# Optimization experiments

Hardware: AMD Instinct MI355X
Metric: run time of the kernel (lower is better)

Reference implementation:

```python
import jax, jax.numpy as jnp
import numpy as np

HIDDEN = 2048
NUM_HEADS = 32
NUM_KV_HEADS = 8
HEAD_DIM = 64
ROPE_THETA = 10000.0


def _rope_tables(S, dtype=jnp.float32):
    freqs = 1.0 / (ROPE_THETA ** (jnp.arange(0, HEAD_DIM, 2, dtype=jnp.float32) / HEAD_DIM))
    angles = jnp.arange(S, dtype=jnp.float32)[:, None] * freqs[None, :]  # [S, D/2]
    return jnp.cos(angles).astype(dtype), jnp.sin(angles).astype(dtype)


def _apply_rope(x, cos, sin):
    # x: [B, H, S, D] with interleaved even/odd rotation pairs
    xe = x[..., 0::2]
    xo = x[..., 1::2]
    oe = xe * cos - xo * sin
    oo = xe * sin + xo * cos
    return jnp.stack([oe, oo], axis=-1).reshape(x.shape)


def setup_inputs() -> dict:
    key = jax.random.key(0)
    ks = jax.random.split(key, 5)
    scale = 0.02
    return {
        "x": jax.random.normal(ks[0], (2, 2048, HIDDEN), dtype=jnp.float32),
        "wq": jax.random.normal(ks[1], (NUM_HEADS * HEAD_DIM, HIDDEN), dtype=jnp.float32) * scale,
        "wk": jax.random.normal(ks[2], (NUM_KV_HEADS * HEAD_DIM, HIDDEN), dtype=jnp.float32) * scale,
        "wv": jax.random.normal(ks[3], (NUM_KV_HEADS * HEAD_DIM, HIDDEN), dtype=jnp.float32) * scale,
        "wo": jax.random.normal(ks[4], (HIDDEN, NUM_HEADS * HEAD_DIM), dtype=jnp.float32) * scale,
    }


def reference(x, wq, wk, wv, wo):
    B, S, _ = x.shape
    G = NUM_HEADS // NUM_KV_HEADS  # GQA group size

    q = (x @ wq.T).reshape(B, S, NUM_HEADS, HEAD_DIM).transpose(0, 2, 1, 3)      # [B,Hq,S,D]
    k = (x @ wk.T).reshape(B, S, NUM_KV_HEADS, HEAD_DIM).transpose(0, 2, 1, 3)   # [B,Hkv,S,D]
    v = (x @ wv.T).reshape(B, S, NUM_KV_HEADS, HEAD_DIM).transpose(0, 2, 1, 3)

    cos, sin = _rope_tables(S, x.dtype)
    q = _apply_rope(q, cos, sin)
    k = _apply_rope(k, cos, sin)

    # GQA without materializing repeated K/V: fold group dim into q
    qg = q.reshape(B, NUM_KV_HEADS, G, S, HEAD_DIM)
    scale = 1.0 / jnp.sqrt(jnp.asarray(HEAD_DIM, dtype=x.dtype))
    scores = jnp.einsum("bkgsd,bktd->bkgst", qg, k) * scale  # [B,Hkv,G,S,S]

    causal = jnp.tril(jnp.ones((S, S), dtype=bool))
    scores = jnp.where(causal, scores, jnp.finfo(scores.dtype).min)
    probs = jax.nn.softmax(scores, axis=-1)

    out = jnp.einsum("bkgst,bktd->bkgsd", probs, v)                 # [B,Hkv,G,S,D]
    out = out.reshape(B, NUM_HEADS, S, HEAD_DIM).transpose(0, 2, 1, 3).reshape(B, S, NUM_HEADS * HEAD_DIM)
    return out @ wo.T
```

## Files before the change

### kernel.cpp

```cpp
#include <hip/hip_runtime.h>
#include <hip/hip_bf16.h>

typedef __hip_bfloat16 bf16;
typedef __attribute__((ext_vector_type(8))) short short8;
typedef __attribute__((ext_vector_type(4))) float f32x4;

#define S_LEN 2048
#define BATCH 2
#define M_TOT 4096
#define HID 2048
#define NH 32
#define NKV 8
#define HD 64
#define KVD 512

#define MFMA16(a, b, c) __builtin_amdgcn_mfma_f32_16x16x32_bf16(a, b, c, 0, 0, 0)

__device__ __forceinline__ void gload_lds16(const bf16* g, bf16* l) {
    __builtin_amdgcn_global_load_lds((const __attribute__((address_space(1))) void*)g,
                                     (__attribute__((address_space(3))) void*)l,
                                     16, 0, 0);
}

__device__ __forceinline__ float b2f(short v) {
    unsigned u = ((unsigned)(unsigned short)v) << 16;
    float f; __builtin_memcpy(&f, &u, 4); return f;
}

__global__ void cast_kernel(const float* __restrict__ src, bf16* __restrict__ dst, int n8) {
    int stride = gridDim.x * blockDim.x;
    for (int i = blockIdx.x * blockDim.x + threadIdx.x; i < n8; i += stride) {
        const float4* s = (const float4*)(src + (size_t)i * 8);
        float4 a = s[0], b = s[1];
        bf16 tmp[8];
        tmp[0] = __float2bfloat16(a.x); tmp[1] = __float2bfloat16(a.y);
        tmp[2] = __float2bfloat16(a.z); tmp[3] = __float2bfloat16(a.w);
        tmp[4] = __float2bfloat16(b.x); tmp[5] = __float2bfloat16(b.y);
        tmp[6] = __float2bfloat16(b.z); tmp[7] = __float2bfloat16(b.w);
        *(short8*)(dst + (size_t)i * 8) = *(short8*)tmp;
    }
}

__global__ void rope_tables_kernel(float* __restrict__ cosb, float* __restrict__ sinb) {
    int idx = blockIdx.x * blockDim.x + threadIdx.x;
    if (idx >= S_LEN * 32) return;
    int s = idx >> 5, d = idx & 31;
    float freq = powf(10000.0f, -(float)(2 * d) / 64.0f);
    float ang = (float)s * freq;
    cosb[idx] = cosf(ang);
    sinb[idx] = sinf(ang);
}

__global__ void rope_kernel(bf16* __restrict__ buf, const float* __restrict__ cosb,
                            const float* __restrict__ sinb, int nh, int npairs) {
    int stride = gridDim.x * blockDim.x;
    int hw = nh * 32;
    for (int idx = blockIdx.x * blockDim.x + threadIdx.x; idx < npairs; idx += stride) {
        int m = idx / hw;
        int r = idx - m * hw;
        int h = r >> 5, d = r & 31;
        int s = m & (S_LEN - 1);
        float c = cosb[s * 32 + d], sn = sinb[s * 32 + d];
        bf16* p = buf + (size_t)m * (nh * HD) + h * HD + 2 * d;
        __hip_bfloat162 xv = *(__hip_bfloat162*)p;
        float xe = __bfloat162float(xv.x), xo = __bfloat162float(xv.y);
        __hip_bfloat162 ov;
        ov.x = __float2bfloat16(xe * c - xo * sn);
        ov.y = __float2bfloat16(xe * sn + xo * c);
        *(__hip_bfloat162*)p = ov;
    }
}

__device__ __forceinline__ short8 rope8(short8 v, float4 c, float4 s) {
    short8 o;
    const float* cp = (const float*)&c;
    const float* sp = (const float*)&s;
    #pragma unroll
    for (int m = 0; m < 4; m++) {
        float xe = b2f(v[2 * m]) * 0.125f;
        float xo = b2f(v[2 * m + 1]) * 0.125f;
        bf16 oe = __float2bfloat16(xe * cp[m] - xo * sp[m]);
        bf16 oo = __float2bfloat16(xe * sp[m] + xo * cp[m]);
        short se, so;
        __builtin_memcpy(&se, &oe, 2); __builtin_memcpy(&so, &oo, 2);
        o[2 * m] = se; o[2 * m + 1] = so;
    }
    return o;
}

__device__ __forceinline__ void gemm_core(const bf16* __restrict__ A,
                                          const bf16* __restrict__ W,
                                          int K, int m0, int n0,
                                          bf16* As, bf16* Bs,
                                          f32x4 acc[4][4]) {
    int tid = threadIdx.x;
    int lane = tid & 63, wid = tid >> 6;
    int wr = wid >> 1, wc = wid & 1;
    int lhi = lane >> 4, llo = lane & 15;
    const bf16* gA[4]; const bf16* gB[4];
    bf16 *lA[4], *lB[4];
    #pragma unroll
    for (int q = 0; q < 4; q++) {
        int c = tid + 256 * q;
        int row = c >> 3;
        int sl = (c & 7) ^ (row & 7);
        gA[q] = A + (size_t)(m0 + row) * K + sl * 8;
        gB[q] = W + (size_t)(n0 + row) * K + sl * 8;
        lA[q] = As + c * 8;
        lB[q] = Bs + c * 8;
    }
    for (int k0 = 0; k0 < K; k0 += 64) {
        #pragma unroll
        for (int q = 0; q < 4; q++) {
            gload_lds16(gA[q] + k0, lA[q]);
            gload_lds16(gB[q] + k0, lB[q]);
        }
        __syncthreads();
        short8 af[4][2], bfr[4][2];
        #pragma unroll
        for (int i = 0; i < 4; i++) {
            int row = wr * 64 + i * 16 + llo;
            int x = row & 7;
            af[i][0] = *(const short8*)(As + row * 64 + ((lhi ^ x) * 8));
            af[i][1] = *(const short8*)(As + row * 64 + (((4 + lhi) ^ x) * 8));
        }
        #pragma unroll
        for (int j = 0; j < 4; j++) {
            int row = wc * 64 + j * 16 + llo;
            int x = row & 7;
            bfr[j][0] = *(const short8*)(Bs + row * 64 + ((lhi ^ x) * 8));
            bfr[j][1] = *(const short8*)(Bs + row * 64 + (((4 + lhi) ^ x) * 8));
        }
        #pragma unroll
        for (int i = 0; i < 4; i++)
            #pragma unroll
            for (int j = 0; j < 4; j++) {
                acc[i][j] = MFMA16(af[i][0], bfr[j][0], acc[i][j]);
                acc[i][j] = MFMA16(af[i][1], bfr[j][1], acc[i][j]);
            }
        __syncthreads();
    }
}

__global__ __launch_bounds__(256) void gemm_qkv_kernel(
        const bf16* __restrict__ xb,
        const bf16* __restrict__ wq, const bf16* __restrict__ wk, const bf16* __restrict__ wv,
        bf16* __restrict__ qb, bf16* __restrict__ kb, bf16* __restrict__ vtb) {
    __shared__ bf16 As[128 * 64];
    __shared__ bf16 Bs[128 * 64];
    int by = blockIdx.y;
    const bf16* W; bf16* Cb; int n0, ldc, mode;
    if (by < 16)      { W = wq; Cb = qb;  n0 = by * 128;        ldc = 2048; mode = 0; }
    else if (by < 20) { W = wk; Cb = kb;  n0 = (by - 16) * 128; ldc = 512;  mode = 0; }
    else              { W = wv; Cb = vtb; n0 = (by - 20) * 128; ldc = 0;    mode = 1; }
    int m0 = blockIdx.x * 128;

    f32x4 acc[4][4] = {};
    gemm_core(xb, W, HID, m0, n0, As, Bs, acc);

    int lane = threadIdx.x & 63, wid = threadIdx.x >> 6;
    int wr = wid >> 1, wc = wid & 1;
    int lhi = lane >> 4, llo = lane & 15;
    #pragma unroll
    for (int i = 0; i < 4; i++)
        #pragma unroll
        for (int j = 0; j < 4; j++) {
            int col = wc * 64 + j * 16 + llo;
            #pragma unroll
            for (int r = 0; r < 4; r++) {
                int row = wr * 64 + i * 16 + lhi * 4 + r;
                int m = m0 + row;
                float v = acc[i][j][r];
                if (mode == 0) {
                    Cb[(size_t)m * ldc + n0 + col] = __float2bfloat16(v);
                } else {
                    int bb = m >> 11, ss = m & 2047;
                    Cb[((size_t)(bb * 512 + n0 + col)) * S_LEN + ss] = __float2bfloat16(v);
                }
            }
        }
}

__global__ __launch_bounds__(256) void gemm_out_kernel(
        const bf16* __restrict__ attnb, const bf16* __restrict__ wob,
        float* __restrict__ out) {
    __shared__ bf16 As[128 * 64];
    __shared__ bf16 Bs[128 * 64];
    int m0 = blockIdx.x * 128;
    int n0 = blockIdx.y * 128;
    f32x4 acc[4][4] = {};
    gemm_core(attnb, wob, HID, m0, n0, As, Bs, acc);

    int lane = threadIdx.x & 63, wid = threadIdx.x >> 6;
    int wr = wid >> 1, wc = wid & 1;
    int lhi = lane >> 4, llo = lane & 15;
    #pragma unroll
    for (int i = 0; i < 4; i++)
        #pragma unroll
        for (int j = 0; j < 4; j++) {
            int col = wc * 64 + j * 16 + llo;
            #pragma unroll
            for (int r = 0; r < 4; r++) {
                int row = wr * 64 + i * 16 + lhi * 4 + r;
                out[(size_t)(m0 + row) * HID + n0 + col] = acc[i][j][r];
            }
        }
}

__global__ __launch_bounds__(256, 4) void flash_kernel(
        const bf16* __restrict__ qb, const bf16* __restrict__ kb,
        const bf16* __restrict__ vtb, const float* __restrict__ cosb,
        const float* __restrict__ sinb, bf16* __restrict__ attnb) {
    __shared__ bf16 Ks[2][64 * 64];
    __shared__ bf16 Vs[2][64 * 64];
    __shared__ bf16 Pl[4][16 * 64];
    int bh = blockIdx.y;
    int b = bh >> 5, h = bh & 31;
    int kvh = h >> 2;
    int tid = threadIdx.x;
    int wid = tid >> 6, lane = tid & 63;
    int lhi = lane >> 4, llo = lane & 15;

    const bf16* Kg = kb + (size_t)(b * S_LEN) * KVD + kvh * HD;
    const bf16* Vg = vtb + (size_t)(b * 512 + kvh * 64) * S_LEN;

    int c0 = tid, c1 = tid + 256;
    int r0 = c0 >> 3, s0 = ((c0 & 7) ^ (r0 & 7)) * 8;
    int r1 = c1 >> 3, s1 = ((c1 & 7) ^ (r1 & 7)) * 8;

    bf16* pl = &Pl[wid][0];
    const int prd0 = llo * 64 + ((lhi ^ (llo & 7)) * 8);
    const int prd1 = llo * 64 + (((lhi + 4) ^ (llo & 7)) * 8);

    auto stage = [&](int buf, int t0) {
        gload_lds16(Kg + (size_t)(t0 + r0) * KVD + s0, &Ks[buf][c0 * 8]);
        gload_lds16(Kg + (size_t)(t0 + r1) * KVD + s1, &Ks[buf][c1 * 8]);
        gload_lds16(Vg + (size_t)r0 * S_LEN + t0 + s0, &Vs[buf][c0 * 8]);
        gload_lds16(Vg + (size_t)r1 * S_LEN + t0 + s1, &Vs[buf][c1 * 8]);
    };

    auto run_phase = [&](int j) {
        int qrow0 = j * 64 + wid * 16;
        int spos = qrow0 + llo;
        const bf16* qrow = qb + ((size_t)(b * S_LEN) + spos) * (NH * HD) + h * HD;
        float4 cv0 = *(const float4*)(cosb + spos * 32 + lhi * 4);
        float4 sv0 = *(const float4*)(sinb + spos * 32 + lhi * 4);
        float4 cv1 = *(const float4*)(cosb + spos * 32 + 16 + lhi * 4);
        float4 sv1 = *(const float4*)(sinb + spos * 32 + 16 + lhi * 4);
        short8 qf0 = rope8(*(const short8*)(qrow + lhi * 8), cv0, sv0);
        short8 qf1 = rope8(*(const short8*)(qrow + 32 + lhi * 8), cv1, sv1);

        f32x4 acc[4] = {};
        float psum[4] = {0.f, 0.f, 0.f, 0.f};

        stage(0, 0);
        asm volatile("s_waitcnt vmcnt(0)" ::: "memory");
        __builtin_amdgcn_s_barrier();
        int cur = 0;
        for (int t = 0; t <= j; ++t) {
            int t0 = t * 64;
            if (t < j) stage(cur ^ 1, t0 + 64);
            const bf16* Kc = &Ks[cur][0];
            const bf16* Vc = &Vs[cur][0];
            f32x4 z[4];
            #pragma unroll
            for (int cb = 0; cb < 4; cb++) {
                int row = cb * 16 + llo;
                int x = row & 7;
                short8 k0 = *(const short8*)(Kc + row * 64 + ((lhi ^ x) * 8));
                short8 k1 = *(const short8*)(Kc + row * 64 + (((lhi + 4) ^ x) * 8));
                f32x4 zz = {0.f, 0.f, 0.f, 0.f};
                zz = MFMA16(qf0, k0, zz);
                zz = MFMA16(qf1, k1, zz);
                z[cb] = zz;
            }
            if (t == j) {
                #pragma unroll
                for (int cb = 0; cb < 4; cb++)
                    #pragma unroll
                    for (int r = 0; r < 4; r++) {
                        float p = __expf(z[cb][r]);
                        p = (t0 + cb * 16 + llo <= qrow0 + lhi * 4 + r) ? p : 0.f;
                        psum[r] += p;
                        int row = lhi * 4 + r;
                        pl[row * 64 + (((2 * cb + (llo >> 3)) ^ (row & 7)) * 8) + (llo & 7)]
                            = __float2bfloat16(p);
                    }
            } else {
                #pragma unroll
                for (int cb = 0; cb < 4; cb++)
                    #pragma unroll
                    for (int r = 0; r < 4; r++) {
                        float p = __expf(z[cb][r]);
                        psum[r] += p;
                        int row = lhi * 4 + r;
                        pl[row * 64 + (((2 * cb + (llo >> 3)) ^ (row & 7)) * 8) + (llo & 7)]
                            = __float2bfloat16(p);
                    }
            }
            short8 pa0 = *(const short8*)(pl + prd0);
            short8 pa1 = *(const short8*)(pl + prd1);
            #pragma unroll
            for (int jb = 0; jb < 4; jb++) {
                int row = jb * 16 + llo;
                int x = row & 7;
                short8 v0 = *(const short8*)(Vc + row * 64 + ((lhi ^ x) * 8));
                short8 v1 = *(const short8*)(Vc + row * 64 + (((lhi + 4) ^ x) * 8));
                acc[jb] = MFMA16(pa0, v0, acc[jb]);
                acc[jb] = MFMA16(pa1, v1, acc[jb]);
            }
            asm volatile("s_waitcnt vmcnt(0)" ::: "memory");
            __builtin_amdgcn_s_barrier();
            cur ^= 1;
        }
        #pragma unroll
        for (int off = 1; off < 16; off <<= 1)
            #pragma unroll
            for (int r = 0; r < 4; r++)
                psum[r] += __shfl_xor(psum[r], off, 64);
        float inv[4];
        #pragma unroll
        for (int r = 0; r < 4; r++) inv[r] = 1.0f / psum[r];
        size_t obase = ((size_t)(b * S_LEN) + qrow0) * (NH * HD) + h * HD;
        #pragma unroll
        for (int jb = 0; jb < 4; jb++)
            #pragma unroll
            for (int r = 0; r < 4; r++)
                attnb[obase + (size_t)(lhi * 4 + r) * (NH * HD) + jb * 16 + llo] =
                    __float2bfloat16(acc[jb][r] * inv[r]);
    };

    run_phase(blockIdx.x);
    run_phase(31 - blockIdx.x);
}

extern "C" void kernel_launch(void* const* d_in, const int* in_sizes, int n_in,
                              void* d_out, int out_size, void* d_ws, size_t ws_size,
                              hipStream_t stream) {
    const float* x  = (const float*)d_in[0];
    const float* wq = (const float*)d_in[1];
    const float* wk = (const float*)d_in[2];
    const float* wv = (const float*)d_in[3];
    const float* wo = (const float*)d_in[4];
    float* out = (float*)d_out;

    char* ws = (char*)d_ws;
    size_t off = 0;
    auto alloc = [&](size_t bytes) { void* p = ws + off; off += (bytes + 255) & ~(size_t)255; return p; };
    bf16* xb   = (bf16*)alloc((size_t)M_TOT * HID * 2);
    bf16* wqb  = (bf16*)alloc((size_t)HID * HID * 2);
    bf16* wkb  = (bf16*)alloc((size_t)512 * HID * 2);
    bf16* wvb  = (bf16*)alloc((size_t)512 * HID * 2);
    bf16* wob  = (bf16*)alloc((size_t)HID * HID * 2);
    bf16* qb   = (bf16*)alloc((size_t)M_TOT * 2048 * 2);
    bf16* kb   = (bf16*)alloc((size_t)M_TOT * 512 * 2);
    bf16* vtb  = (bf16*)alloc((size_t)M_TOT * 512 * 2);
    bf16* attnb= (bf16*)alloc((size_t)M_TOT * 2048 * 2);
    float* cosb= (float*)alloc((size_t)S_LEN * 32 * 4);
    float* sinb= (float*)alloc((size_t)S_LEN * 32 * 4);

    auto cast = [&](const float* s, bf16* d, int n) {
        int n8 = n / 8;
        int grid = (n8 + 255) / 256;
        cast_kernel<<<grid, 256, 0, stream>>>(s, d, n8);
    };
    cast(x,  xb,  M_TOT * HID);
    cast(wq, wqb, HID * HID);
    cast(wk, wkb, 512 * HID);
    cast(wv, wvb, 512 * HID);
    cast(wo, wob, HID * HID);

    rope_tables_kernel<<<(S_LEN * 32 + 255) / 256, 256, 0, stream>>>(cosb, sinb);

    gemm_qkv_kernel<<<dim3(M_TOT / 128, 24), 256, 0, stream>>>(xb, wqb, wkb, wvb, qb, kb, vtb);

    {
        int npairs = M_TOT * NKV * 32;
        rope_kernel<<<(npairs + 255) / 256, 256, 0, stream>>>(kb, cosb, sinb, NKV, npairs);
    }

    flash_kernel<<<dim3(16, BATCH * NH), 256, 0, stream>>>(qb, kb, vtb, cosb, sinb, attnb);

    gemm_out_kernel<<<dim3(M_TOT / 128, HID / 128), 256, 0, stream>>>(attnb, wob, out);
}
```

Before: 211.9 us.

## Double-buffer GEMM K-loop, swizzle block order, fuse input casts into one kernel

The shared GEMM core now uses a K-step of 32 with two LDS buffers, issuing the next tile's global-to-LDS loads before the current tile's MFMAs. This overlaps memory latency with compute and leaves one barrier per step. Both GEMM kernels remap blockIdx.x so consecutive blocks walk strided M tiles, which changes cache locality. The five fp32-to-bf16 cast launches are merged into one grid-stride kernel writing into a contiguous workspace. That merge relies on the bf16 buffers being allocated contiguously with no alignment padding between them, and the smaller K-step doubles the number of loop iterations and barriers.

```diff
diff --git a/kernel.cpp b/kernel.cpp
--- a/kernel.cpp
+++ b/kernel.cpp
@@ -27,11 +27,23 @@
     float f; __builtin_memcpy(&f, &u, 4); return f;
 }
 
-__global__ void cast_kernel(const float* __restrict__ src, bf16* __restrict__ dst, int n8) {
+#define N8_X   1048576
+#define N8_WQ   524288
+#define N8_WK   131072
+#define N8_TOT 2359296
+__global__ void cast_all_kernel(const float* __restrict__ x, const float* __restrict__ wq,
+                                const float* __restrict__ wk, const float* __restrict__ wv,
+                                const float* __restrict__ wo, bf16* __restrict__ dst) {
     int stride = gridDim.x * blockDim.x;
-    for (int i = blockIdx.x * blockDim.x + threadIdx.x; i < n8; i += stride) {
-        const float4* s = (const float4*)(src + (size_t)i * 8);
-        float4 a = s[0], b = s[1];
+    for (int i = blockIdx.x * blockDim.x + threadIdx.x; i < N8_TOT; i += stride) {
+        const float* s; int off;
+        if (i < N8_X)                        { s = x;  off = i; }
+        else if (i < N8_X + N8_WQ)           { s = wq; off = i - N8_X; }
+        else if (i < N8_X + N8_WQ + N8_WK)   { s = wk; off = i - (N8_X + N8_WQ); }
+        else if (i < N8_X + N8_WQ + 2*N8_WK) { s = wv; off = i - (N8_X + N8_WQ + N8_WK); }
+        else                                 { s = wo; off = i - (N8_X + N8_WQ + 2*N8_WK); }
+        const float4* sp = (const float4*)(s + (size_t)off * 8);
+        float4 a = sp[0], b = sp[1];
         bf16 tmp[8];
         tmp[0] = __float2bfloat16(a.x); tmp[1] = __float2bfloat16(a.y);
         tmp[2] = __float2bfloat16(a.z); tmp[3] = __float2bfloat16(a.w);
@@ -97,48 +109,50 @@
     int lane = tid & 63, wid = tid >> 6;
     int wr = wid >> 1, wc = wid & 1;
     int lhi = lane >> 4, llo = lane & 15;
-    const bf16* gA[4]; const bf16* gB[4];
-    bf16 *lA[4], *lB[4];
-    #pragma unroll
-    for (int q = 0; q < 4; q++) {
-        int c = tid + 256 * q;
-        int row = c >> 3;
-        int sl = (c & 7) ^ (row & 7);
-        gA[q] = A + (size_t)(m0 + row) * K + sl * 8;
-        gB[q] = W + (size_t)(n0 + row) * K + sl * 8;
-        lA[q] = As + c * 8;
-        lB[q] = Bs + c * 8;
-    }
-    for (int k0 = 0; k0 < K; k0 += 64) {
-        #pragma unroll
-        for (int q = 0; q < 4; q++) {
-            gload_lds16(gA[q] + k0, lA[q]);
-            gload_lds16(gB[q] + k0, lB[q]);
-        }
-        __syncthreads();
-        short8 af[4][2], bfr[4][2];
+    int c0 = tid, c1 = tid + 256;
+    int r0 = c0 >> 2, s0 = ((c0 & 3) ^ (r0 & 3)) * 8;
+    int r1 = c1 >> 2, s1 = ((c1 & 3) ^ (r1 & 3)) * 8;
+    const bf16* gA0 = A + (size_t)(m0 + r0) * K + s0;
+    const bf16* gA1 = A + (size_t)(m0 + r1) * K + s1;
+    const bf16* gB0 = W + (size_t)(n0 + r0) * K + s0;
+    const bf16* gB1 = W + (size_t)(n0 + r1) * K + s1;
+
+    auto stage = [&](int buf, int k0) {
+        bf16* a = As + buf * 4096;
+        bf16* b = Bs + buf * 4096;
+        gload_lds16(gA0 + k0, a + c0 * 8);
+        gload_lds16(gA1 + k0, a + c1 * 8);
+        gload_lds16(gB0 + k0, b + c0 * 8);
+        gload_lds16(gB1 + k0, b + c1 * 8);
+    };
+
+    stage(0, 0);
+    asm volatile("s_waitcnt vmcnt(0)" ::: "memory");
+    __builtin_amdgcn_s_barrier();
+    int buf = 0;
+    for (int k0 = 0; k0 < K; k0 += 32) {
+        if (k0 + 32 < K) stage(buf ^ 1, k0 + 32);
+        const bf16* Ac = As + buf * 4096;
+        const bf16* Bc = Bs + buf * 4096;
+        short8 af[4], bfr[4];
         #pragma unroll
         for (int i = 0; i < 4; i++) {
             int row = wr * 64 + i * 16 + llo;
-            int x = row & 7;
-            af[i][0] = *(const short8*)(As + row * 64 + ((lhi ^ x) * 8));
-            af[i][1] = *(const short8*)(As + row * 64 + (((4 + lhi) ^ x) * 8));
+            af[i] = *(const short8*)(Ac + row * 32 + ((lhi ^ (row & 3)) * 8));
         }
         #pragma unroll
         for (int j = 0; j < 4; j++) {
             int row = wc * 64 + j * 16 + llo;
-            int x = row & 7;
-            bfr[j][0] = *(const short8*)(Bs + row * 64 + ((lhi ^ x) * 8));
-            bfr[j][1] = *(const short8*)(Bs + row * 64 + (((4 + lhi) ^ x) * 8));
+            bfr[j] = *(const short8*)(Bc + row * 32 + ((lhi ^ (row & 3)) * 8));
         }
         #pragma unroll
         for (int i = 0; i < 4; i++)
             #pragma unroll
-            for (int j = 0; j < 4; j++) {
-                acc[i][j] = MFMA16(af[i][0], bfr[j][0], acc[i][j]);
-                acc[i][j] = MFMA16(af[i][1], bfr[j][1], acc[i][j]);
-            }
-        __syncthreads();
+            for (int j = 0; j < 4; j++)
+                acc[i][j] = MFMA16(af[i], bfr[j], acc[i][j]);
+        asm volatile("s_waitcnt vmcnt(0)" ::: "memory");
+        __builtin_amdgcn_s_barrier();
+        buf ^= 1;
     }
 }
 
@@ -146,14 +160,16 @@
         const bf16* __restrict__ xb,
         const bf16* __restrict__ wq, const bf16* __restrict__ wk, const bf16* __restrict__ wv,
         bf16* __restrict__ qb, bf16* __restrict__ kb, bf16* __restrict__ vtb) {
-    __shared__ bf16 As[128 * 64];
-    __shared__ bf16 Bs[128 * 64];
+    __shared__ bf16 As[2 * 128 * 32];
+    __shared__ bf16 Bs[2 * 128 * 32];
     int by = blockIdx.y;
     const bf16* W; bf16* Cb; int n0, ldc, mode;
     if (by < 16)      { W = wq; Cb = qb;  n0 = by * 128;        ldc = 2048; mode = 0; }
     else if (by < 20) { W = wk; Cb = kb;  n0 = (by - 16) * 128; ldc = 512;  mode = 0; }
     else              { W = wv; Cb = vtb; n0 = (by - 20) * 128; ldc = 0;    mode = 1; }
-    int m0 = blockIdx.x * 128;
+    int bx = blockIdx.x;
+    int bxs = (bx & 7) * 4 + (bx >> 3);
+    int m0 = bxs * 128;
 
     f32x4 acc[4][4] = {};
     gemm_core(xb, W, HID, m0, n0, As, Bs, acc);
@@ -184,9 +200,11 @@
 __global__ __launch_bounds__(256) void gemm_out_kernel(
         const bf16* __restrict__ attnb, const bf16* __restrict__ wob,
         float* __restrict__ out) {
-    __shared__ bf16 As[128 * 64];
-    __shared__ bf16 Bs[128 * 64];
-    int m0 = blockIdx.x * 128;
+    __shared__ bf16 As[2 * 128 * 32];
+    __shared__ bf16 Bs[2 * 128 * 32];
+    int bx = blockIdx.x;
+    int bxs = (bx & 7) * 4 + (bx >> 3);
+    int m0 = bxs * 128;
     int n0 = blockIdx.y * 128;
     f32x4 acc[4][4] = {};
     gemm_core(attnb, wob, HID, m0, n0, As, Bs, acc);
@@ -359,16 +377,7 @@
     float* cosb= (float*)alloc((size_t)S_LEN * 32 * 4);
     float* sinb= (float*)alloc((size_t)S_LEN * 32 * 4);
 
-    auto cast = [&](const float* s, bf16* d, int n) {
-        int n8 = n / 8;
-        int grid = (n8 + 255) / 256;
-        cast_kernel<<<grid, 256, 0, stream>>>(s, d, n8);
-    };
-    cast(x,  xb,  M_TOT * HID);
-    cast(wq, wqb, HID * HID);
-    cast(wk, wkb, 512 * HID);
-    cast(wv, wvb, 512 * HID);
-    cast(wo, wob, HID * HID);
+    cast_all_kernel<<<2048, 256, 0, stream>>>(x, wq, wk, wv, wo, xb);
 
     rope_tables_kernel<<<(S_LEN * 32 + 255) / 256, 256, 0, stream>>>(cosb, sinb);
 
```

After: 215.0 us. Within noise of the previous version (+1.5%).
